# Performance work log

Hardware: AMD Instinct MI355X
Metric: run time of the kernel (lower is better)

Reference implementation:

```python
import jax, jax.numpy as jnp
import numpy as np

B, N, DEG, EMB = 8, 256, 16, 64
E = B * N * DEG  # 32768 edges

RB_KEYS = ("rb_m1w1", "rb_m1b1", "rb_m1w2", "rb_m1b2",
           "rb_m2w1", "rb_m2b1", "rb_m2w2", "rb_m2b2", "rb_sw", "rb_sb")


def setup_inputs() -> dict:
    key = jax.random.key(0)
    ks = jax.random.split(key, 32)
    # equal-size graphs: graph g owns global nodes [g*N, (g+1)*N)
    gid = jnp.repeat(jnp.arange(B, dtype=jnp.int32), N * DEG)
    src = gid * N + jax.random.randint(ks[0], (E,), 0, N, dtype=jnp.int32)
    dst = gid * N + jax.random.randint(ks[1], (E,), 0, N, dtype=jnp.int32)
    edge_index = jnp.stack([src, dst])  # [2, E] int32
    batch = jnp.repeat(jnp.arange(B, dtype=jnp.int32), N)  # [B*N]

    def mk(k, shape):
        return (jax.random.normal(k, shape) * 0.1).astype(jnp.float32)

    inp = {"edge_index": edge_index, "batch": batch}
    inp.update(dict(
        rb0_m1w1=mk(ks[2], (EMB, 2)), rb0_m1b1=mk(ks[3], (EMB,)),
        rb0_m1w2=mk(ks[4], (EMB, EMB)), rb0_m1b2=mk(ks[5], (EMB,)),
        rb0_m2w1=mk(ks[6], (EMB, 2)), rb0_m2b1=mk(ks[7], (EMB,)),
        rb0_m2w2=mk(ks[8], (EMB, EMB)), rb0_m2b2=mk(ks[9], (EMB,)),
        rb0_sw=mk(ks[10], (EMB, 2 + EMB)), rb0_sb=mk(ks[11], (EMB,)),
        rb_m1w1=mk(ks[12], (3, EMB, EMB)), rb_m1b1=mk(ks[13], (3, EMB)),
        rb_m1w2=mk(ks[14], (3, EMB, EMB)), rb_m1b2=mk(ks[15], (3, EMB)),
        rb_m2w1=mk(ks[16], (3, EMB, EMB)), rb_m2b1=mk(ks[17], (3, EMB)),
        rb_m2w2=mk(ks[18], (3, EMB, EMB)), rb_m2b2=mk(ks[19], (3, EMB)),
        rb_sw=mk(ks[20], (3, EMB, 2 * EMB)), rb_sb=mk(ks[21], (3, EMB)),
        fcw1=mk(ks[22], (EMB, 2 * EMB)), fcb1=mk(ks[23], (EMB,)),
        fcw2=mk(ks[24], (1, EMB)), fcb2=mk(ks[25], (1,)),
    ))
    return inp


def _conv1x1(z, W, b):  # z: [B,Cin,N,N], W: [Cout,Cin]
    return jnp.einsum('oc,bcij->boij', W, z) + b[None, :, None, None]


def _regular_block(z, p):
    (m1w1, m1b1, m1w2, m1b2, m2w1, m2b1, m2w2, m2b2, sw, sb) = p
    m1 = jax.nn.relu(_conv1x1(jax.nn.relu(_conv1x1(z, m1w1, m1b1)), m1w2, m1b2))
    m2 = jax.nn.relu(_conv1x1(jax.nn.relu(_conv1x1(z, m2w1, m2b1)), m2w2, m2b2))
    mult = jnp.einsum('bcij,bcjk->bcik', m1, m2)  # per-channel NxN matmul
    return _conv1x1(jnp.concatenate([z, mult], axis=1), sw, sb)  # skip


def _forward(edge_index, batch, p):
    # to_dense_adj: scatter edges into [B,N,N]
    gid = batch[edge_index[0]]
    lu = edge_index[0] - gid * N
    lv = edge_index[1] - gid * N
    adj = jnp.zeros((B, N, N), jnp.float32).at[gid, lu, lv].add(1.0)
    # channels: [dense_edge_data, diag(zero node embedding)] -> [B,2,N,N]
    z = jnp.stack([adj, jnp.zeros_like(adj)], axis=1)
    z = _regular_block(z, (p['rb0_m1w1'], p['rb0_m1b1'], p['rb0_m1w2'], p['rb0_m1b2'],
                           p['rb0_m2w1'], p['rb0_m2b1'], p['rb0_m2w2'], p['rb0_m2b2'],
                           p['rb0_sw'], p['rb0_sb']))
    for i in range(3):
        z = _regular_block(z, tuple(p[k][i] for k in RB_KEYS))
    # diag_offdiag_meanpool, graph level -> [B, 2C]
    diag = jnp.diagonal(z, axis1=-2, axis2=-1)  # [B,C,N]
    mean_diag = diag.mean(-1)
    mean_off = (z.sum((-2, -1)) - diag.sum(-1)) / (N * (N - 1))
    h = jnp.concatenate([mean_diag, mean_off], axis=1)
    h = jax.nn.relu(h @ p['fcw1'].T + p['fcb1'])
    return h @ p['fcw2'].T + p['fcb2']  # [B,1]


def reference(edge_index, batch,
              rb0_m1w1, rb0_m1b1, rb0_m1w2, rb0_m1b2,
              rb0_m2w1, rb0_m2b1, rb0_m2w2, rb0_m2b2, rb0_sw, rb0_sb,
              rb_m1w1, rb_m1b1, rb_m1w2, rb_m1b2,
              rb_m2w1, rb_m2b1, rb_m2w2, rb_m2b2, rb_sw, rb_sb,
              fcw1, fcb1, fcw2, fcb2):
    p = dict(rb0_m1w1=rb0_m1w1, rb0_m1b1=rb0_m1b1, rb0_m1w2=rb0_m1w2, rb0_m1b2=rb0_m1b2,
             rb0_m2w1=rb0_m2w1, rb0_m2b1=rb0_m2b1, rb0_m2w2=rb0_m2w2, rb0_m2b2=rb0_m2b2,
             rb0_sw=rb0_sw, rb0_sb=rb0_sb,
             rb_m1w1=rb_m1w1, rb_m1b1=rb_m1b1, rb_m1w2=rb_m1w2, rb_m1b2=rb_m1b2,
             rb_m2w1=rb_m2w1, rb_m2b1=rb_m2b1, rb_m2w2=rb_m2w2, rb_m2b2=rb_m2b2,
             rb_sw=rb_sw, rb_sb=rb_sb, fcw1=fcw1, fcb1=fcb1, fcw2=fcw2, fcb2=fcb2)
    return _forward(edge_index, batch, p)
```

## Files before the change

kernel.cpp:

```cpp
#include <hip/hip_runtime.h>

#define N 256
#define NN 65536
#define EMB 64
#define BATCH 8
#define NEDGE 32768

typedef unsigned short u16;
typedef unsigned int u32t;
typedef __attribute__((ext_vector_type(8))) short bf16x8;
typedef __attribute__((ext_vector_type(4))) float f32x4;

#define TSTR 72

#define RB0_W2A 0
#define RB0_W2B 4096
#define RB0_SW  8192
#define REG_BASE 12288
#define REG_STRIDE 24576
#define WSPLIT_ELEMS 86016

static __device__ __forceinline__ u16 f2bs(float f) {
    u32t u = __float_as_uint(f);
    u32t r = (u + 0x7FFFu + ((u >> 16) & 1u)) >> 16;
    return (u16)r;
}
static __device__ __forceinline__ float b2f(u16 s) {
    return __uint_as_float(((u32t)s) << 16);
}
static __device__ __forceinline__ void split_bf(float a, u16& hi, u16& lo) {
    hi = f2bs(a);
    float r = a - b2f(hi);
    lo = f2bs(r);
}

__global__ void scatter_adj(const int* __restrict__ ei, const int* __restrict__ batch,
                            float* __restrict__ adj) {
    int e = blockIdx.x * blockDim.x + threadIdx.x;
    if (e >= NEDGE) return;
    int src = ei[e];
    int dst = ei[NEDGE + e];
    int g = batch[src];
    int lu = src - g * N;
    int lv = dst - g * N;
    atomicAdd(&adj[(size_t)g * NN + (size_t)lu * N + lv], 1.0f);
}

__global__ void prep_w(const float* __restrict__ rb0_m1w2, const float* __restrict__ rb0_m2w2,
                       const float* __restrict__ rb0_sw,
                       const float* __restrict__ rb_m1w1, const float* __restrict__ rb_m1w2,
                       const float* __restrict__ rb_m2w1, const float* __restrict__ rb_m2w2,
                       const float* __restrict__ rb_sw,
                       u16* __restrict__ wh, u16* __restrict__ wl) {
    int idx = blockIdx.x * 256 + threadIdx.x;
    if (idx >= WSPLIT_ELEMS) return;
    float v;
    if (idx < 4096) v = rb0_m1w2[idx];
    else if (idx < 8192) v = rb0_m2w2[idx - 4096];
    else if (idx < 12288) { int e = idx - 8192; v = rb0_sw[(e >> 6) * 66 + 2 + (e & 63)]; }
    else {
        int e = idx - REG_BASE;
        int blk = e / REG_STRIDE, r = e % REG_STRIDE;
        if (r < 4096) v = rb_m1w1[blk * 4096 + r];
        else if (r < 8192) v = rb_m1w2[blk * 4096 + r - 4096];
        else if (r < 12288) v = rb_m2w1[blk * 4096 + r - 8192];
        else if (r < 16384) v = rb_m2w2[blk * 4096 + r - 12288];
        else v = rb_sw[blk * 8192 + r - 16384];
    }
    u16 h, l;
    split_bf(v, h, l);
    wh[idx] = h; wl[idx] = l;
}


__device__ __forceinline__ void stage_w64(const u16* __restrict__ Wh, const u16* __restrict__ Wl,
                                          u16* dh, u16* dl, int t) {
#pragma unroll
    for (int it = 0; it < 2; ++it) {
        int idx = it * 256 + t;
        int row = idx >> 3, g = idx & 7;
        int4 vh = *(const int4*)&Wh[row * 64 + g * 8];
        int4 vl = *(const int4*)&Wl[row * 64 + g * 8];
        int d = row * 64 + ((g ^ (row & 7)) << 3);
        *(int4*)&dh[d] = vh;
        *(int4*)&dl[d] = vl;
    }
}
__device__ __forceinline__ void stage_w128s(const u16* __restrict__ Wh, const u16* __restrict__ Wl,
                                            u16* dh, u16* dl, int t) {
#pragma unroll
    for (int it = 0; it < 4; ++it) {
        int idx = it * 256 + t;
        int row = idx >> 4, g = idx & 15;
        int4 vh = *(const int4*)&Wh[row * 128 + g * 8];
        int4 vl = *(const int4*)&Wl[row * 128 + g * 8];
        int d = row * 128 + ((g ^ (row & 7)) << 3);
        *(int4*)&dh[d] = vh;
        *(int4*)&dl[d] = vl;
    }
}
__device__ __forceinline__ bf16x8 wfrag64(const u16* w, int row, int k0) {
    int g = k0 >> 3;
    return *(const bf16x8*)&w[row * 64 + ((g ^ (row & 7)) << 3)];
}
__device__ __forceinline__ bf16x8 wfrag128(const u16* w, int row, int k0) {
    int g = k0 >> 3;
    return *(const bf16x8*)&w[row * 128 + ((g ^ (row & 7)) << 3)];
}

__device__ __forceinline__ void stage_act_nchw(const float* __restrict__ src, int p0,
                                               u16* ah, u16* al, int t) {
#pragma unroll
    for (int it = 0; it < 8; ++it) {
        int idx = it * 256 + t;
        int px = idx & 63;
        int c0 = (idx >> 6) * 2;
        float v0 = src[(size_t)c0 * NN + p0 + px];
        float v1 = src[(size_t)(c0 + 1) * NN + p0 + px];
        u16 h0, l0, h1, l1;
        split_bf(v0, h0, l0); split_bf(v1, h1, l1);
        *(u32t*)&ah[px * TSTR + c0] = (u32t)h0 | ((u32t)h1 << 16);
        *(u32t*)&al[px * TSTR + c0] = (u32t)l0 | ((u32t)l1 << 16);
    }
}
__device__ __forceinline__ void stage_band_nchw(const float* __restrict__ src, int p0,
                                                u16* ah, u16* al, int wband, int lane) {
    int q = lane >> 4, l15 = lane & 15;
    int px = wband * 16 + l15;
    int gpx = p0 + px;
#pragma unroll
    for (int it = 0; it < 8; ++it) {
        int c0 = it * 8 + q * 2;
        float v0 = src[(size_t)c0 * NN + gpx];
        float v1 = src[(size_t)(c0 + 1) * NN + gpx];
        u16 h0, l0, h1, l1;
        split_bf(v0, h0, l0); split_bf(v1, h1, l1);
        *(u32t*)&ah[px * TSTR + c0] = (u32t)h0 | ((u32t)h1 << 16);
        *(u32t*)&al[px * TSTR + c0] = (u32t)l0 | ((u32t)l1 << 16);
    }
}

__device__ __forceinline__ void zfrags_nchw(const float* __restrict__ zp, int px,
                                            int q, bf16x8 zfh[2], bf16x8 zfl[2]) {
#pragma unroll
    for (int ks = 0; ks < 2; ++ks)
#pragma unroll
        for (int j = 0; j < 8; ++j) {
            float v = zp[(size_t)(ks * 32 + q * 8 + j) * NN + px];
            u16 h, l; split_bf(v, h, l);
            zfh[ks][j] = (short)h;
            zfl[ks][j] = (short)l;
        }
}

__device__ __forceinline__ void init_bias(const float* __restrict__ Bb, f32x4* acc, int lane) {
    int q = lane >> 4;
#pragma unroll
    for (int ot = 0; ot < 4; ++ot)
#pragma unroll
        for (int j = 0; j < 4; ++j)
            acc[ot][j] = Bb[ot * 16 + q * 4 + j];
}

__device__ __forceinline__ void mfma_L1_64(bf16x8 zfh[2], bf16x8 zfl[2],
                                           const u16* wh, const u16* wl,
                                           f32x4* acc, int lane) {
    int q = lane >> 4, l = lane & 15;
#pragma unroll
    for (int ks = 0; ks < 2; ++ks) {
        int k0 = ks * 32 + q * 8;
#pragma unroll
        for (int ot = 0; ot < 4; ++ot) {
            bf16x8 ahi = wfrag64(wh, ot * 16 + l, k0);
            bf16x8 alo = wfrag64(wl, ot * 16 + l, k0);
            acc[ot] = __builtin_amdgcn_mfma_f32_16x16x32_bf16(ahi, zfh[ks], acc[ot], 0, 0, 0);
            acc[ot] = __builtin_amdgcn_mfma_f32_16x16x32_bf16(ahi, zfl[ks], acc[ot], 0, 0, 0);
            acc[ot] = __builtin_amdgcn_mfma_f32_16x16x32_bf16(alo, zfh[ks], acc[ot], 0, 0, 0);
        }
    }
}
__device__ __forceinline__ void mfma_L1_128(bf16x8 zfh[2], bf16x8 zfl[2],
                                            const u16* wh, const u16* wl, int ak0,
                                            f32x4* acc, int lane) {
    int q = lane >> 4, l = lane & 15;
#pragma unroll
    for (int ks = 0; ks < 2; ++ks) {
        int k0 = ks * 32 + q * 8;
#pragma unroll
        for (int ot = 0; ot < 4; ++ot) {
            bf16x8 ahi = wfrag128(wh, ot * 16 + l, ak0 + k0);
            bf16x8 alo = wfrag128(wl, ot * 16 + l, ak0 + k0);
            acc[ot] = __builtin_amdgcn_mfma_f32_16x16x32_bf16(ahi, zfh[ks], acc[ot], 0, 0, 0);
            acc[ot] = __builtin_amdgcn_mfma_f32_16x16x32_bf16(ahi, zfl[ks], acc[ot], 0, 0, 0);
            acc[ot] = __builtin_amdgcn_mfma_f32_16x16x32_bf16(alo, zfh[ks], acc[ot], 0, 0, 0);
        }
    }
}

__device__ __forceinline__ void layer_h2(const u16* hbuf,
                                         const u16* wh, const u16* wl,
                                         f32x4* acc, int wv, int lane) {
    int q = lane >> 4, l = lane & 15;
#pragma unroll
    for (int ks = 0; ks < 2; ++ks) {
        int k0 = ks * 32 + q * 8;
        bf16x8 b = wfrag64(hbuf, wv * 16 + l, k0);
#pragma unroll
        for (int ot = 0; ot < 4; ++ot) {
            bf16x8 ahi = wfrag64(wh, ot * 16 + l, k0);
            bf16x8 alo = wfrag64(wl, ot * 16 + l, k0);
            acc[ot] = __builtin_amdgcn_mfma_f32_16x16x32_bf16(ahi, b, acc[ot], 0, 0, 0);
            acc[ot] = __builtin_amdgcn_mfma_f32_16x16x32_bf16(alo, b, acc[ot], 0, 0, 0);
        }
    }
}
__device__ __forceinline__ void layer_half128(const u16* bh, const u16* bl,
                                              const u16* wh, const u16* wl, int ak0,
                                              f32x4* acc, int wv, int lane) {
    int q = lane >> 4, l = lane & 15;
#pragma unroll
    for (int ks = 0; ks < 2; ++ks) {
        int k0 = ks * 32 + q * 8;
        int boff = (wv * 16 + l) * TSTR + k0;
        bf16x8 bhi = *(const bf16x8*)&bh[boff];
        bf16x8 blo = *(const bf16x8*)&bl[boff];
#pragma unroll
        for (int ot = 0; ot < 4; ++ot) {
            bf16x8 ahi = wfrag128(wh, ot * 16 + l, ak0 + k0);
            bf16x8 alo = wfrag128(wl, ot * 16 + l, ak0 + k0);
            acc[ot] = __builtin_amdgcn_mfma_f32_16x16x32_bf16(ahi, bhi, acc[ot], 0, 0, 0);
            acc[ot] = __builtin_amdgcn_mfma_f32_16x16x32_bf16(ahi, blo, acc[ot], 0, 0, 0);
            acc[ot] = __builtin_amdgcn_mfma_f32_16x16x32_bf16(alo, bhi, acc[ot], 0, 0, 0);
        }
    }
}
__device__ __forceinline__ void layer_half64(const u16* bh, const u16* bl,
                                             const u16* wh, const u16* wl,
                                             f32x4* acc, int wv, int lane) {
    int q = lane >> 4, l = lane & 15;
#pragma unroll
    for (int ks = 0; ks < 2; ++ks) {
        int k0 = ks * 32 + q * 8;
        int boff = (wv * 16 + l) * TSTR + k0;
        bf16x8 bhi = *(const bf16x8*)&bh[boff];
        bf16x8 blo = *(const bf16x8*)&bl[boff];
#pragma unroll
        for (int ot = 0; ot < 4; ++ot) {
            bf16x8 ahi = wfrag64(wh, ot * 16 + l, k0);
            bf16x8 alo = wfrag64(wl, ot * 16 + l, k0);
            acc[ot] = __builtin_amdgcn_mfma_f32_16x16x32_bf16(ahi, bhi, acc[ot], 0, 0, 0);
            acc[ot] = __builtin_amdgcn_mfma_f32_16x16x32_bf16(ahi, blo, acc[ot], 0, 0, 0);
            acc[ot] = __builtin_amdgcn_mfma_f32_16x16x32_bf16(alo, bhi, acc[ot], 0, 0, 0);
        }
    }
}

__device__ __forceinline__ void write_h_bf16(f32x4* acc, u16* hbuf, int wv, int lane) {
    int q = lane >> 4, l = lane & 15;
    int px = wv * 16 + l;
#pragma unroll
    for (int ot = 0; ot < 4; ++ot) {
#pragma unroll
        for (int jp = 0; jp < 2; ++jp) {
            int o = ot * 16 + q * 4 + jp * 2;
            int gaddr = px * 64 + (((o >> 3) ^ (px & 7)) << 3) + (o & 7);
            float v0 = acc[ot][jp * 2];     v0 = v0 > 0.f ? v0 : 0.f;
            float v1 = acc[ot][jp * 2 + 1]; v1 = v1 > 0.f ? v1 : 0.f;
            *(u32t*)&hbuf[gaddr] = (u32t)f2bs(v0) | ((u32t)f2bs(v1) << 16);
        }
    }
}

__device__ __forceinline__ void write_m_bf16(f32x4* acc, u16* __restrict__ mh,
                                             int p0, int wv, int lane) {
    int q = lane >> 4, l = lane & 15;
    int px = p0 + wv * 16 + l;
#pragma unroll
    for (int ot = 0; ot < 4; ++ot)
#pragma unroll
        for (int j = 0; j < 4; ++j) {
            int o = ot * 16 + q * 4 + j;
            float v = acc[ot][j]; v = v > 0.f ? v : 0.f;
            mh[(size_t)o * NN + px] = f2bs(v);
        }
}

__device__ __forceinline__ void write_m_lin(f32x4* acc, float* __restrict__ mout,
                                            int p0, int wv, int lane) {
    int q = lane >> 4, l = lane & 15;
    int px = p0 + wv * 16 + l;
#pragma unroll
    for (int ot = 0; ot < 4; ++ot)
#pragma unroll
        for (int j = 0; j < 4; ++j) {
            int o = ot * 16 + q * 4 + j;
            mout[(size_t)o * NN + px] = acc[ot][j];
        }
}

__global__ __launch_bounds__(256, 4) void f1_reg(
    const float* __restrict__ z,
    const u16* __restrict__ wsh, const u16* __restrict__ wsl, int blk,
    const float* __restrict__ B1a, const float* __restrict__ B2a,
    const float* __restrict__ B1b, const float* __restrict__ B2b,
    u16* __restrict__ m1, u16* __restrict__ m2) {
    __shared__ u16 w1h[4096], w1l[4096], w2h[4096], w2l[4096];
    __shared__ u16 hbuf[4096];
    int bb = blockIdx.y, p0 = blockIdx.x * 64;
    int t = threadIdx.x, lane = t & 63, wv = t >> 6;
    int q = lane >> 4, l15 = lane & 15;
    size_t gofs = (size_t)bb * EMB * NN;
    const float* zp = z + gofs;
    const u16* Wbh = wsh + REG_BASE + blk * REG_STRIDE;
    const u16* Wbl = wsl + REG_BASE + blk * REG_STRIDE;

    bf16x8 zfh[2], zfl[2];
    zfrags_nchw(zp, p0 + wv * 16 + l15, q, zfh, zfl);

    stage_w64(Wbh, Wbl, w1h, w1l, t);
    stage_w64(Wbh + 4096, Wbl + 4096, w2h, w2l, t);
    __syncthreads();

    f32x4 acc[4];
    init_bias(B1a, acc, lane);
    mfma_L1_64(zfh, zfl, w1h, w1l, acc, lane);
    write_h_bf16(acc, hbuf, wv, lane);
    init_bias(B2a, acc, lane);
    layer_h2(hbuf, w2h, w2l, acc, wv, lane);
    write_m_bf16(acc, m1 + gofs, p0, wv, lane);

    __syncthreads();
    stage_w64(Wbh + 8192, Wbl + 8192, w1h, w1l, t);
    stage_w64(Wbh + 12288, Wbl + 12288, w2h, w2l, t);
    __syncthreads();

    init_bias(B1b, acc, lane);
    mfma_L1_64(zfh, zfl, w1h, w1l, acc, lane);
    write_h_bf16(acc, hbuf, wv, lane);
    init_bias(B2b, acc, lane);
    layer_h2(hbuf, w2h, w2l, acc, wv, lane);
    write_m_bf16(acc, m2 + gofs, p0, wv, lane);
}

__global__ __launch_bounds__(256, 4) void f1_rb0(
    const float* __restrict__ adj, int b_base,
    const float* __restrict__ w1a, const float* __restrict__ b1a,
    const float* __restrict__ w1b, const float* __restrict__ b1b,
    const u16* __restrict__ wsh, const u16* __restrict__ wsl,
    const float* __restrict__ B2a, const float* __restrict__ B2b,
    u16* __restrict__ m1, u16* __restrict__ m2) {
    __shared__ u16 w1h[4096], w1l[4096], w2h[4096], w2l[4096];
    __shared__ u16 hbuf[4096];
    int bb = blockIdx.y, p0 = blockIdx.x * 64;
    int t = threadIdx.x, lane = t & 63, wv = t >> 6;
    int q = lane >> 4, l15 = lane & 15;
    size_t gofs = (size_t)bb * EMB * NN;
    int pxl = wv * 16 + l15;
    float a = adj[(size_t)(b_base + bb) * NN + p0 + pxl];

    stage_w64(wsh + RB0_W2A, wsl + RB0_W2A, w1h, w1l, t);
    stage_w64(wsh + RB0_W2B, wsl + RB0_W2B, w2h, w2l, t);
#pragma unroll
    for (int it = 0; it < 8; ++it) {
        int o0 = it * 8 + q * 2;
        int gaddr = pxl * 64 + ((it ^ (pxl & 7)) << 3) + q * 2;
        float v0 = w1a[o0 * 2] * a + b1a[o0];             v0 = v0 > 0.f ? v0 : 0.f;
        float v1 = w1a[(o0 + 1) * 2] * a + b1a[o0 + 1];   v1 = v1 > 0.f ? v1 : 0.f;
        *(u32t*)&hbuf[gaddr] = (u32t)f2bs(v0) | ((u32t)f2bs(v1) << 16);
    }
    __syncthreads();

    f32x4 acc[4];
    init_bias(B2a, acc, lane);
    layer_h2(hbuf, w1h, w1l, acc, wv, lane);
    write_m_bf16(acc, m1 + gofs, p0, wv, lane);

#pragma unroll
    for (int it = 0; it < 8; ++it) {
        int o0 = it * 8 + q * 2;
        int gaddr = pxl * 64 + ((it ^ (pxl & 7)) << 3) + q * 2;
        float v0 = w1b[o0 * 2] * a + b1b[o0];             v0 = v0 > 0.f ? v0 : 0.f;
        float v1 = w1b[(o0 + 1) * 2] * a + b1b[o0 + 1];   v1 = v1 > 0.f ? v1 : 0.f;
        *(u32t*)&hbuf[gaddr] = (u32t)f2bs(v0) | ((u32t)f2bs(v1) << 16);
    }
    init_bias(B2b, acc, lane);
    layer_h2(hbuf, w2h, w2l, acc, wv, lane);
    write_m_bf16(acc, m2 + gofs, p0, wv, lane);
}

__device__ __forceinline__ int soff(int row, int g) {
    return row * 64 + ((g ^ (row & 7) ^ ((row >> 3) & 7)) << 3);
}

__global__ __launch_bounds__(512) void chanmm_mfma(
    const u16* __restrict__ m1, const u16* __restrict__ m2,
    float* __restrict__ mult) {
    __shared__ u16 Ah[128 * 64];
    __shared__ u16 Bh[64 * 64];
    int t = threadIdx.x, lane = t & 63, wv = t >> 6;
    int l15 = lane & 15, q = lane >> 4;
    int wi = wv >> 1, wj = wv & 1;
    int tile = blockIdx.x;
    int itile = (tile >> 2) * 128, jtile = (tile & 3) * 64;
    int ch = blockIdx.y, bb = blockIdx.z;
    size_t pb = ((size_t)bb * EMB + ch) * NN;
    const u16* A_h = m1 + pb;
    const u16* B_h = m2 + pb;

    int a_i = t >> 3;
    int a_g = t & 7;
    int b_k = t >> 3;
    int b_j8 = (t & 7) * 8;

    int4 rAh0, rAh1, rBh;
#define LOADK(K0)                                                              \
    {                                                                          \
        int k0_ = (K0);                                                        \
        rAh0 = *(const int4*)&A_h[(itile + a_i) * N + k0_ + a_g * 8];          \
        rAh1 = *(const int4*)&A_h[(itile + 64 + a_i) * N + k0_ + a_g * 8];     \
        rBh  = *(const int4*)&B_h[(k0_ + b_k) * N + jtile + b_j8];             \
    }

    f32x4 acc[2][2] = {};
    LOADK(0);
#pragma unroll
    for (int s = 0; s < 4; ++s) {
        *(int4*)&Ah[soff(a_i, a_g)] = rAh0;
        *(int4*)&Ah[soff(a_i + 64, a_g)] = rAh1;
        {
            const u16* ph = (const u16*)&rBh;
            int G = b_k >> 3, kin = b_k & 7;
#pragma unroll
            for (int d = 0; d < 8; ++d) {
                int j = b_j8 + d;
                Bh[soff(j, G) + kin] = ph[d];
            }
        }
        __syncthreads();
        if (s < 3) LOADK((s + 1) * 64);
#pragma unroll
        for (int ks = 0; ks < 2; ++ks) {
            int g = ks * 4 + q;
            bf16x8 bhi[2];
#pragma unroll
            for (int jt = 0; jt < 2; ++jt) {
                int rj = wj * 32 + jt * 16 + l15;
                bhi[jt] = *(const bf16x8*)&Bh[soff(rj, g)];
            }
#pragma unroll
            for (int it = 0; it < 2; ++it) {
                int ri = wi * 32 + it * 16 + l15;
                bf16x8 ahi = *(const bf16x8*)&Ah[soff(ri, g)];
#pragma unroll
                for (int jt = 0; jt < 2; ++jt)
                    acc[it][jt] = __builtin_amdgcn_mfma_f32_16x16x32_bf16(ahi, bhi[jt], acc[it][jt], 0, 0, 0);
            }
        }
        __syncthreads();
    }
#undef LOADK
    float* O = mult + pb;
#pragma unroll
    for (int it = 0; it < 2; ++it)
#pragma unroll
        for (int jt = 0; jt < 2; ++jt)
#pragma unroll
            for (int r = 0; r < 4; ++r) {
                int i = itile + wi * 32 + it * 16 + q * 4 + r;
                int j = jtile + wj * 32 + jt * 16 + l15;
                O[(size_t)i * N + j] = acc[it][jt][r];
            }
}

__global__ __launch_bounds__(256, 3) void f2_reg(
    const float* __restrict__ mult,
    const u16* __restrict__ wsh, const u16* __restrict__ wsl, int blk,
    const float* __restrict__ SB,
    float* __restrict__ z) {
    __shared__ u16 wh[8192], wl[8192];
    __shared__ u16 ah[64 * TSTR], al[64 * TSTR];
    int bb = blockIdx.y, p0 = blockIdx.x * 64;
    int t = threadIdx.x, lane = t & 63, wv = t >> 6;
    int q = lane >> 4, l15 = lane & 15;
    const float* mp = mult + (size_t)bb * EMB * NN;
    float* zp = z + (size_t)bb * EMB * NN;
    const u16* SWh = wsh + REG_BASE + blk * REG_STRIDE + 16384;
    const u16* SWl = wsl + REG_BASE + blk * REG_STRIDE + 16384;

    bf16x8 zfh[2], zfl[2];
    zfrags_nchw(zp, p0 + wv * 16 + l15, q, zfh, zfl);

    stage_w128s(SWh, SWl, wh, wl, t);
    stage_band_nchw(mp, p0, ah, al, wv, lane);
    __syncthreads();

    f32x4 acc[4];
    init_bias(SB, acc, lane);
    mfma_L1_128(zfh, zfl, wh, wl, 0, acc, lane);
    layer_half128(ah, al, wh, wl, 64, acc, wv, lane);
    write_m_lin(acc, zp, p0, wv, lane);
}

__global__ __launch_bounds__(256, 3) void f2_rb0(
    const float* __restrict__ adj, int b_base,
    const float* __restrict__ mult,
    const u16* __restrict__ wsh, const u16* __restrict__ wsl,
    const float* __restrict__ SWf, const float* __restrict__ SB,
    float* __restrict__ z) {
    __shared__ u16 ah[64 * TSTR], al[64 * TSTR];
    __shared__ u16 wh[4096], wl[4096];
    int bb = blockIdx.y, p0 = blockIdx.x * 64;
    int t = threadIdx.x, lane = t & 63, wv = t >> 6;
    const float* mp = mult + (size_t)bb * EMB * NN;
    float* zp = z + (size_t)bb * EMB * NN;

    stage_w64(wsh + RB0_SW, wsl + RB0_SW, wh, wl, t);
    stage_act_nchw(mp, p0, ah, al, t);
    __syncthreads();

    int q = lane >> 4, l = lane & 15;
    float a = adj[(size_t)(b_base + bb) * NN + p0 + wv * 16 + l];
    f32x4 acc[4];
#pragma unroll
    for (int ot = 0; ot < 4; ++ot)
#pragma unroll
        for (int j = 0; j < 4; ++j) {
            int o = ot * 16 + q * 4 + j;
            acc[ot][j] = SB[o] + SWf[o * 66] * a;
        }
    layer_half64(ah, al, wh, wl, acc, wv, lane);
    write_m_lin(acc, zp, p0, wv, lane);
}

__global__ void pool(const float* __restrict__ z, float* __restrict__ sums, int b_base) {
    int bb = blockIdx.x;
    int c = blockIdx.y;
    size_t base = ((size_t)bb * EMB + c) * NN;
    const float4* z4 = (const float4*)(z + base);
    int t = threadIdx.x;
    float s = 0.0f;
#pragma unroll 4
    for (int it = 0; it < 64; ++it) {
        float4 v = z4[it * 256 + t];
        s += v.x + v.y + v.z + v.w;
    }
    float d = z[base + (size_t)t * 257];
    for (int off = 32; off > 0; off >>= 1) {
        s += __shfl_down(s, off);
        d += __shfl_down(d, off);
    }
    __shared__ float ls[4], ld[4];
    int wid = t >> 6;
    if ((t & 63) == 0) { ls[wid] = s; ld[wid] = d; }
    __syncthreads();
    if (t == 0) {
        s = ls[0] + ls[1] + ls[2] + ls[3];
        d = ld[0] + ld[1] + ld[2] + ld[3];
        int b = b_base + bb;
        sums[b * EMB + c] = s;
        sums[BATCH * EMB + b * EMB + c] = d;
    }
}

__global__ void fc(const float* __restrict__ sums,
                   const float* __restrict__ fcw1, const float* __restrict__ fcb1,
                   const float* __restrict__ fcw2, const float* __restrict__ fcb2,
                   float* __restrict__ out) {
    int b = blockIdx.x;
    __shared__ float h[128];
    __shared__ float hh2[64];
    int t = threadIdx.x;
    if (t < 64) {
        h[t] = sums[BATCH * EMB + b * EMB + t] / (float)N;
    } else {
        int c = t - 64;
        float sall = sums[b * EMB + c];
        float sd = sums[BATCH * EMB + b * EMB + c];
        h[t] = (sall - sd) / (float)(N * (N - 1));
    }
    __syncthreads();
    if (t < 64) {
        float acc = fcb1[t];
        for (int k = 0; k < 128; ++k) acc += fcw1[t * 128 + k] * h[k];
        hh2[t] = acc > 0.0f ? acc : 0.0f;
    }
    __syncthreads();
    if (t == 0) {
        float acc = fcb2[0];
        for (int k = 0; k < 64; ++k) acc += fcw2[k] * hh2[k];
        out[b] = acc;
    }
}

extern "C" void kernel_launch(void* const* d_in, const int* in_sizes, int n_in,
                              void* d_out, int out_size, void* d_ws, size_t ws_size,
                              hipStream_t stream) {
    const int* ei       = (const int*)d_in[0];
    const int* batchv   = (const int*)d_in[1];
    const float* rb0_m1w1 = (const float*)d_in[2];
    const float* rb0_m1b1 = (const float*)d_in[3];
    const float* rb0_m1w2 = (const float*)d_in[4];
    const float* rb0_m1b2 = (const float*)d_in[5];
    const float* rb0_m2w1 = (const float*)d_in[6];
    const float* rb0_m2b1 = (const float*)d_in[7];
    const float* rb0_m2w2 = (const float*)d_in[8];
    const float* rb0_m2b2 = (const float*)d_in[9];
    const float* rb0_sw   = (const float*)d_in[10];
    const float* rb0_sb   = (const float*)d_in[11];
    const float* rb_m1w1  = (const float*)d_in[12];
    const float* rb_m1b1  = (const float*)d_in[13];
    const float* rb_m1w2  = (const float*)d_in[14];
    const float* rb_m1b2  = (const float*)d_in[15];
    const float* rb_m2w1  = (const float*)d_in[16];
    const float* rb_m2b1  = (const float*)d_in[17];
    const float* rb_m2w2  = (const float*)d_in[18];
    const float* rb_m2b2  = (const float*)d_in[19];
    const float* rb_sw    = (const float*)d_in[20];
    const float* rb_sb    = (const float*)d_in[21];
    const float* fcw1     = (const float*)d_in[22];
    const float* fcb1     = (const float*)d_in[23];
    const float* fcw2     = (const float*)d_in[24];
    const float* fcb2     = (const float*)d_in[25];

    const size_t P = (size_t)EMB * NN;
    const size_t WB = (size_t)WSPLIT_ELEMS * 2ull;
    const size_t fixedBytes = 524288ull * 4ull + 4096ull + 2ull * WB;
    const size_t perGraphBytes = 2ull * P * 2ull + P * 4ull + P * 4ull;
    int g = BATCH;
    while (g > 1) {
        if (fixedBytes + (size_t)g * perGraphBytes <= ws_size) break;
        g >>= 1;
    }

    char* w = (char*)d_ws;
    float* adj   = (float*)w;  w += 524288ull * 4ull;
    float* sums  = (float*)w;  w += 4096;
    u16* wsh     = (u16*)w;    w += WB;
    u16* wsl     = (u16*)w;    w += WB;
    u16* m1      = (u16*)w;    w += (size_t)g * P * 2ull;
    u16* m2      = (u16*)w;    w += (size_t)g * P * 2ull;
    float* mult  = (float*)w;  w += (size_t)g * P * 4ull;
    float* znchw = (float*)w;  w += (size_t)g * P * 4ull;

    hipMemsetAsync(adj, 0, 524288ull * 4ull, stream);
    scatter_adj<<<NEDGE / 256, 256, 0, stream>>>(ei, batchv, adj);
    prep_w<<<(WSPLIT_ELEMS + 255) / 256, 256, 0, stream>>>(
        rb0_m1w2, rb0_m2w2, rb0_sw, rb_m1w1, rb_m1w2, rb_m2w1, rb_m2w2, rb_sw, wsh, wsl);

    for (int b_base = 0; b_base < BATCH; b_base += g) {
        dim3 gridE(NN / 64, g);
        dim3 gridM(8, EMB, g);

        f1_rb0<<<gridE, 256, 0, stream>>>(adj, b_base,
            rb0_m1w1, rb0_m1b1, rb0_m2w1, rb0_m2b1,
            wsh, wsl, rb0_m1b2, rb0_m2b2, m1, m2);
        chanmm_mfma<<<gridM, 512, 0, stream>>>(m1, m2, mult);
        f2_rb0<<<gridE, 256, 0, stream>>>(adj, b_base, mult, wsh, wsl, rb0_sw, rb0_sb, znchw);

        for (int i = 0; i < 3; ++i) {
            f1_reg<<<gridE, 256, 0, stream>>>(znchw, wsh, wsl, i,
                rb_m1b1 + i * 64, rb_m1b2 + i * 64,
                rb_m2b1 + i * 64, rb_m2b2 + i * 64,
                m1, m2);
            chanmm_mfma<<<gridM, 512, 0, stream>>>(m1, m2, mult);
            f2_reg<<<gridE, 256, 0, stream>>>(mult, wsh, wsl, i, rb_sb + i * 64, znchw);
        }

        pool<<<dim3(g, EMB), 256, 0, stream>>>(znchw, sums, b_base);
    }
    fc<<<BATCH, 128, 0, stream>>>(sums, fcw1, fcb1, fcw2, fcb2, (float*)d_out);
}
```

Measured before the change: 924.4 us.

## Store channel-matmul output in bf16 and drop hi/lo split for skip conv

The per-channel matmul result is now written as a single bf16 value instead of fp32, which halves its global write and read traffic. The skip-conv kernels read it directly into a swizzled LDS tile and use two MFMAs per step (weights split hi/lo, activation single) instead of three. The smaller LDS footprint lets the launch bounds request 4 blocks per CU. The cost is lower precision on the mult tensor, since its low-order bits are discarded, which could affect accuracy.

```diff
diff --git a/kernel.cpp b/kernel.cpp
--- a/kernel.cpp
+++ b/kernel.cpp
@@ -10,8 +10,6 @@
 typedef unsigned int u32t;
 typedef __attribute__((ext_vector_type(8))) short bf16x8;
 typedef __attribute__((ext_vector_type(4))) float f32x4;
-
-#define TSTR 72
 
 #define RB0_W2A 0
 #define RB0_W2B 4096
@@ -108,35 +106,31 @@
     return *(const bf16x8*)&w[row * 128 + ((g ^ (row & 7)) << 3)];
 }
 
-__device__ __forceinline__ void stage_act_nchw(const float* __restrict__ src, int p0,
-                                               u16* ah, u16* al, int t) {
+__device__ __forceinline__ void stage_band_m(const u16* __restrict__ src, int p0,
+                                             u16* mb, int wband, int lane) {
+    int q = lane >> 4, l15 = lane & 15;
+    int px = wband * 16 + l15;
+    int gpx = p0 + px;
+#pragma unroll
+    for (int it = 0; it < 8; ++it) {
+        int c0 = it * 8 + q * 2;
+        u16 v0 = src[(size_t)c0 * NN + gpx];
+        u16 v1 = src[(size_t)(c0 + 1) * NN + gpx];
+        int gaddr = px * 64 + ((it ^ (px & 7)) << 3) + q * 2;
+        *(u32t*)&mb[gaddr] = (u32t)v0 | ((u32t)v1 << 16);
+    }
+}
+__device__ __forceinline__ void stage_act_m(const u16* __restrict__ src, int p0,
+                                            u16* mb, int t) {
 #pragma unroll
     for (int it = 0; it < 8; ++it) {
         int idx = it * 256 + t;
         int px = idx & 63;
         int c0 = (idx >> 6) * 2;
-        float v0 = src[(size_t)c0 * NN + p0 + px];
-        float v1 = src[(size_t)(c0 + 1) * NN + p0 + px];
-        u16 h0, l0, h1, l1;
-        split_bf(v0, h0, l0); split_bf(v1, h1, l1);
-        *(u32t*)&ah[px * TSTR + c0] = (u32t)h0 | ((u32t)h1 << 16);
-        *(u32t*)&al[px * TSTR + c0] = (u32t)l0 | ((u32t)l1 << 16);
-    }
-}
-__device__ __forceinline__ void stage_band_nchw(const float* __restrict__ src, int p0,
-                                                u16* ah, u16* al, int wband, int lane) {
-    int q = lane >> 4, l15 = lane & 15;
-    int px = wband * 16 + l15;
-    int gpx = p0 + px;
-#pragma unroll
-    for (int it = 0; it < 8; ++it) {
-        int c0 = it * 8 + q * 2;
-        float v0 = src[(size_t)c0 * NN + gpx];
-        float v1 = src[(size_t)(c0 + 1) * NN + gpx];
-        u16 h0, l0, h1, l1;
-        split_bf(v0, h0, l0); split_bf(v1, h1, l1);
-        *(u32t*)&ah[px * TSTR + c0] = (u32t)h0 | ((u32t)h1 << 16);
-        *(u32t*)&al[px * TSTR + c0] = (u32t)l0 | ((u32t)l1 << 16);
+        u16 v0 = src[(size_t)c0 * NN + p0 + px];
+        u16 v1 = src[(size_t)(c0 + 1) * NN + p0 + px];
+        int gaddr = px * 64 + ((((c0 >> 3) ^ (px & 7))) << 3) + (c0 & 7);
+        *(u32t*)&mb[gaddr] = (u32t)v0 | ((u32t)v1 << 16);
     }
 }
 
@@ -214,43 +208,37 @@
         }
     }
 }
-__device__ __forceinline__ void layer_half128(const u16* bh, const u16* bl,
-                                              const u16* wh, const u16* wl, int ak0,
-                                              f32x4* acc, int wv, int lane) {
+__device__ __forceinline__ void layer_m2_128(const u16* mb,
+                                             const u16* wh, const u16* wl,
+                                             f32x4* acc, int wv, int lane) {
     int q = lane >> 4, l = lane & 15;
 #pragma unroll
     for (int ks = 0; ks < 2; ++ks) {
         int k0 = ks * 32 + q * 8;
-        int boff = (wv * 16 + l) * TSTR + k0;
-        bf16x8 bhi = *(const bf16x8*)&bh[boff];
-        bf16x8 blo = *(const bf16x8*)&bl[boff];
+        bf16x8 b = wfrag64(mb, wv * 16 + l, k0);
 #pragma unroll
         for (int ot = 0; ot < 4; ++ot) {
-            bf16x8 ahi = wfrag128(wh, ot * 16 + l, ak0 + k0);
-            bf16x8 alo = wfrag128(wl, ot * 16 + l, ak0 + k0);
-            acc[ot] = __builtin_amdgcn_mfma_f32_16x16x32_bf16(ahi, bhi, acc[ot], 0, 0, 0);
-            acc[ot] = __builtin_amdgcn_mfma_f32_16x16x32_bf16(ahi, blo, acc[ot], 0, 0, 0);
-            acc[ot] = __builtin_amdgcn_mfma_f32_16x16x32_bf16(alo, bhi, acc[ot], 0, 0, 0);
-        }
-    }
-}
-__device__ __forceinline__ void layer_half64(const u16* bh, const u16* bl,
-                                             const u16* wh, const u16* wl,
-                                             f32x4* acc, int wv, int lane) {
+            bf16x8 ahi = wfrag128(wh, ot * 16 + l, 64 + k0);
+            bf16x8 alo = wfrag128(wl, ot * 16 + l, 64 + k0);
+            acc[ot] = __builtin_amdgcn_mfma_f32_16x16x32_bf16(ahi, b, acc[ot], 0, 0, 0);
+            acc[ot] = __builtin_amdgcn_mfma_f32_16x16x32_bf16(alo, b, acc[ot], 0, 0, 0);
+        }
+    }
+}
+__device__ __forceinline__ void layer_m2_64(const u16* mb,
+                                            const u16* wh, const u16* wl,
+                                            f32x4* acc, int wv, int lane) {
     int q = lane >> 4, l = lane & 15;
 #pragma unroll
     for (int ks = 0; ks < 2; ++ks) {
         int k0 = ks * 32 + q * 8;
-        int boff = (wv * 16 + l) * TSTR + k0;
-        bf16x8 bhi = *(const bf16x8*)&bh[boff];
-        bf16x8 blo = *(const bf16x8*)&bl[boff];
+        bf16x8 b = wfrag64(mb, wv * 16 + l, k0);
 #pragma unroll
         for (int ot = 0; ot < 4; ++ot) {
             bf16x8 ahi = wfrag64(wh, ot * 16 + l, k0);
             bf16x8 alo = wfrag64(wl, ot * 16 + l, k0);
-            acc[ot] = __builtin_amdgcn_mfma_f32_16x16x32_bf16(ahi, bhi, acc[ot], 0, 0, 0);
-            acc[ot] = __builtin_amdgcn_mfma_f32_16x16x32_bf16(ahi, blo, acc[ot], 0, 0, 0);
-            acc[ot] = __builtin_amdgcn_mfma_f32_16x16x32_bf16(alo, bhi, acc[ot], 0, 0, 0);
+            acc[ot] = __builtin_amdgcn_mfma_f32_16x16x32_bf16(ahi, b, acc[ot], 0, 0, 0);
+            acc[ot] = __builtin_amdgcn_mfma_f32_16x16x32_bf16(alo, b, acc[ot], 0, 0, 0);
         }
     }
 }
@@ -394,7 +382,7 @@
 
 __global__ __launch_bounds__(512) void chanmm_mfma(
     const u16* __restrict__ m1, const u16* __restrict__ m2,
-    float* __restrict__ mult) {
+    u16* __restrict__ mult) {
     __shared__ u16 Ah[128 * 64];
     __shared__ u16 Bh[64 * 64];
     int t = threadIdx.x, lane = t & 63, wv = t >> 6;
@@ -459,7 +447,7 @@
         __syncthreads();
     }
 #undef LOADK
-    float* O = mult + pb;
+    u16* O = mult + pb;
 #pragma unroll
     for (int it = 0; it < 2; ++it)
 #pragma unroll
@@ -468,21 +456,21 @@
             for (int r = 0; r < 4; ++r) {
                 int i = itile + wi * 32 + it * 16 + q * 4 + r;
                 int j = jtile + wj * 32 + jt * 16 + l15;
-                O[(size_t)i * N + j] = acc[it][jt][r];
+                O[(size_t)i * N + j] = f2bs(acc[it][jt][r]);
             }
 }
 
-__global__ __launch_bounds__(256, 3) void f2_reg(
-    const float* __restrict__ mult,
+__global__ __launch_bounds__(256, 4) void f2_reg(
+    const u16* __restrict__ mult,
     const u16* __restrict__ wsh, const u16* __restrict__ wsl, int blk,
     const float* __restrict__ SB,
     float* __restrict__ z) {
     __shared__ u16 wh[8192], wl[8192];
-    __shared__ u16 ah[64 * TSTR], al[64 * TSTR];
+    __shared__ u16 mb[4096];
     int bb = blockIdx.y, p0 = blockIdx.x * 64;
     int t = threadIdx.x, lane = t & 63, wv = t >> 6;
     int q = lane >> 4, l15 = lane & 15;
-    const float* mp = mult + (size_t)bb * EMB * NN;
+    const u16* mp = mult + (size_t)bb * EMB * NN;
     float* zp = z + (size_t)bb * EMB * NN;
     const u16* SWh = wsh + REG_BASE + blk * REG_STRIDE + 16384;
     const u16* SWl = wsl + REG_BASE + blk * REG_STRIDE + 16384;
@@ -491,31 +479,31 @@
     zfrags_nchw(zp, p0 + wv * 16 + l15, q, zfh, zfl);
 
     stage_w128s(SWh, SWl, wh, wl, t);
-    stage_band_nchw(mp, p0, ah, al, wv, lane);
+    stage_band_m(mp, p0, mb, wv, lane);
     __syncthreads();
 
     f32x4 acc[4];
     init_bias(SB, acc, lane);
     mfma_L1_128(zfh, zfl, wh, wl, 0, acc, lane);
-    layer_half128(ah, al, wh, wl, 64, acc, wv, lane);
+    layer_m2_128(mb, wh, wl, acc, wv, lane);
     write_m_lin(acc, zp, p0, wv, lane);
 }
 
-__global__ __launch_bounds__(256, 3) void f2_rb0(
+__global__ __launch_bounds__(256, 4) void f2_rb0(
     const float* __restrict__ adj, int b_base,
-    const float* __restrict__ mult,
+    const u16* __restrict__ mult,
     const u16* __restrict__ wsh, const u16* __restrict__ wsl,
     const float* __restrict__ SWf, const float* __restrict__ SB,
     float* __restrict__ z) {
-    __shared__ u16 ah[64 * TSTR], al[64 * TSTR];
     __shared__ u16 wh[4096], wl[4096];
+    __shared__ u16 mb[4096];
     int bb = blockIdx.y, p0 = blockIdx.x * 64;
     int t = threadIdx.x, lane = t & 63, wv = t >> 6;
-    const float* mp = mult + (size_t)bb * EMB * NN;
+    const u16* mp = mult + (size_t)bb * EMB * NN;
     float* zp = z + (size_t)bb * EMB * NN;
 
     stage_w64(wsh + RB0_SW, wsl + RB0_SW, wh, wl, t);
-    stage_act_nchw(mp, p0, ah, al, t);
+    stage_act_m(mp, p0, mb, t);
     __syncthreads();
 
     int q = lane >> 4, l = lane & 15;
@@ -528,7 +516,7 @@
             int o = ot * 16 + q * 4 + j;
             acc[ot][j] = SB[o] + SWf[o * 66] * a;
         }
-    layer_half64(ah, al, wh, wl, acc, wv, lane);
+    layer_m2_64(mb, wh, wl, acc, wv, lane);
     write_m_lin(acc, zp, p0, wv, lane);
 }
 
@@ -625,7 +613,7 @@
     const size_t P = (size_t)EMB * NN;
     const size_t WB = (size_t)WSPLIT_ELEMS * 2ull;
     const size_t fixedBytes = 524288ull * 4ull + 4096ull + 2ull * WB;
-    const size_t perGraphBytes = 2ull * P * 2ull + P * 4ull + P * 4ull;
+    const size_t perGraphBytes = 2ull * P * 2ull + P * 2ull + P * 4ull;
     int g = BATCH;
     while (g > 1) {
         if (fixedBytes + (size_t)g * perGraphBytes <= ws_size) break;
@@ -639,7 +627,7 @@
     u16* wsl     = (u16*)w;    w += WB;
     u16* m1      = (u16*)w;    w += (size_t)g * P * 2ull;
     u16* m2      = (u16*)w;    w += (size_t)g * P * 2ull;
-    float* mult  = (float*)w;  w += (size_t)g * P * 4ull;
+    u16* mult    = (u16*)w;    w += (size_t)g * P * 2ull;
     float* znchw = (float*)w;  w += (size_t)g * P * 4ull;
 
     hipMemsetAsync(adj, 0, 524288ull * 4ull, stream);
```

New measurement: 851.3 us. 1.09x faster.
